# Kernel tuning notes

Measured on AMD Instinct MI355X. Metric: run time of the kernel, lower is better.

## Reference

```python
import jax, jax.numpy as jnp
import numpy as np

N = 100000          # total nodes
G = 128             # number of graphs
D_IN, D_H, D_OUT = 512, 1024, 512
E = 1600000         # edges (unused by the math, matches forward signature)


def setup_inputs() -> dict:
    key = jax.random.key(0)
    ks = jax.random.split(key, 9)
    x = jax.random.normal(ks[0], (N, D_IN), dtype=jnp.float32)
    edge_index = jax.random.randint(ks[1], (2, E), 0, N, dtype=jnp.int64)
    # sorted batch ids; guarantee every graph id appears at least once
    batch = jnp.sort(jnp.concatenate([
        jnp.arange(G, dtype=jnp.int64),
        jax.random.randint(ks[2], (N - G,), 0, G, dtype=jnp.int64),
    ]))
    s = 0.02
    W0 = jax.random.normal(ks[3], (D_IN, D_H), dtype=jnp.float32) * s
    b0 = jnp.zeros((D_H,), dtype=jnp.float32)
    W1 = jax.random.normal(ks[4], (D_H, D_H), dtype=jnp.float32) * s
    b1 = jnp.zeros((D_H,), dtype=jnp.float32)
    W2 = jax.random.normal(ks[5], (D_H, D_OUT), dtype=jnp.float32) * s
    b2 = jnp.zeros((D_OUT,), dtype=jnp.float32)
    return {"x": x, "edge_index": edge_index, "batch": batch,
            "W0": W0, "b0": b0, "W1": W1, "b1": b1, "W2": W2, "b2": b2}


def reference(x, edge_index, batch, W0, b0, W1, b1, W2, b2):
    # Linear + ReLU stack (dropout p=0 -> identity in eval). edge_index is unused,
    # matching the original module (its 'GCN' layer is a plain nn.Linear).
    h = jax.nn.relu(x @ W0 + b0)
    h = jax.nn.relu(h @ W1 + b1)
    h = jax.nn.relu(h @ W2 + b2)        # [N, D_OUT]
    # global mean pool per graph: fused segment-sum replaces the per-graph mask loop
    sums = jax.ops.segment_sum(h, batch, num_segments=G)                 # [G, D_OUT]
    counts = jax.ops.segment_sum(jnp.ones((h.shape[0],), h.dtype), batch,
                                 num_segments=G)                          # [G]
    return sums / counts[:, None]
```

## Files before the change

kernel.cpp:

```cpp
#include <hip/hip_runtime.h>
#include <cstdint>
#include <cstddef>

typedef __bf16 bf16x8 __attribute__((ext_vector_type(8)));
typedef float f32x4 __attribute__((ext_vector_type(4)));

__device__ __forceinline__ unsigned short f2bf(float f) {
  unsigned u = __float_as_uint(f);
  u += 0x7fffu + ((u >> 16) & 1u);
  return (unsigned short)(u >> 16);
}
__device__ __forceinline__ float bf2f(unsigned short s) {
  return __uint_as_float(((unsigned)s) << 16);
}

__device__ __forceinline__ void gld_lds16(const void* g, void* l) {
  __builtin_amdgcn_global_load_lds(
      (const __attribute__((address_space(1))) void*)g,
      (__attribute__((address_space(3))) void*)l, 16, 0, 0);
}

#define BARM() do { __builtin_amdgcn_s_barrier(); asm volatile("" ::: "memory"); } while (0)
#define VMCNT(n) asm volatile("s_waitcnt vmcnt(" #n ")" ::: "memory")

__global__ void transpose_w(const float* __restrict__ w, unsigned short* __restrict__ wt,
                            int K, int N) {
  __shared__ float tile[32][33];
  int nt = N >> 5;
  int bx = blockIdx.x % nt;
  int by = blockIdx.x / nt;
  int tx = threadIdx.x & 31, ty = threadIdx.x >> 5;
#pragma unroll
  for (int r = 0; r < 32; r += 8)
    tile[ty + r][tx] = w[(size_t)(by * 32 + ty + r) * N + bx * 32 + tx];
  __syncthreads();
#pragma unroll
  for (int r = 0; r < 32; r += 8)
    wt[(size_t)(bx * 32 + ty + r) * K + by * 32 + tx] = f2bf(tile[tx][ty + r]);
}

__global__ void cvt_x(const float* __restrict__ x, unsigned short* __restrict__ xb,
                      int rows, int nvalid, int D) {
  size_t total = (size_t)rows * D / 8;
  for (size_t i = (size_t)blockIdx.x * blockDim.x + threadIdx.x; i < total;
       i += (size_t)gridDim.x * blockDim.x) {
    size_t e = i * 8;
    int row = (int)(e / (size_t)D);
    uint4 ov;
    if (row < nvalid) {
      const float4* s = (const float4*)(x + e);
      float4 v0 = s[0], v1 = s[1];
      ov.x = (unsigned)f2bf(v0.x) | ((unsigned)f2bf(v0.y) << 16);
      ov.y = (unsigned)f2bf(v0.z) | ((unsigned)f2bf(v0.w) << 16);
      ov.z = (unsigned)f2bf(v1.x) | ((unsigned)f2bf(v1.y) << 16);
      ov.w = (unsigned)f2bf(v1.z) | ((unsigned)f2bf(v1.w) << 16);
    } else {
      ov.x = ov.y = ov.z = ov.w = 0u;
    }
    *(uint4*)(xb + e) = ov;
  }
}

__device__ __forceinline__ bf16x8 read_frag(const unsigned short* region, int row, int kel) {
  int ke = kel ^ (((row >> 1) & 3) << 3);
  return *(const bf16x8*)(region + row * 32 + ke);
}

__device__ __forceinline__ void stage_half(const unsigned short* gpanel, int K, int kofs,
                                           unsigned short* region, int tid) {
#pragma unroll
  for (int r = 0; r < 2; ++r) {
    int row = r * 128 + (tid >> 2);
    int ke = ((tid & 3) * 8) ^ (((row >> 1) & 3) << 3);
    gld_lds16(gpanel + (size_t)row * K + kofs + ke, region + r * 4096 + tid * 8);
  }
}

#define MFMA16(MB, BV)                                                          \
  do {                                                                          \
    __builtin_amdgcn_s_setprio(1);                                              \
    _Pragma("unroll") for (int mm = 0; mm < 4; ++mm) {                          \
      _Pragma("unroll") for (int nn = 0; nn < 4; ++nn)                          \
        acc[(MB) + mm][nn] = __builtin_amdgcn_mfma_f32_16x16x32_bf16(           \
            av[mm], BV[nn], acc[(MB) + mm][nn], 0, 0, 0);                       \
    }                                                                           \
    __builtin_amdgcn_s_setprio(0);                                              \
  } while (0)

__global__ __launch_bounds__(512, 2) void gemm256(
    const unsigned short* __restrict__ A,
    const unsigned short* __restrict__ Bt,
    const float* __restrict__ bias,
    unsigned short* __restrict__ C,
    int N, int K) {
  __shared__ alignas(16) unsigned short lds[2][2][2][256][32];
  const int tid = threadIdx.x;
  const int w = tid >> 6, l = tid & 63;
  const int wm = w >> 2, wn = w & 3;
  const int lc = l & 15, lk8 = (l >> 4) * 8;

  const int nbn = N >> 8;
  const int nwg = gridDim.x;
  const int q = nwg >> 3, rr = nwg & 7;
  const int xcd = blockIdx.x & 7, ib = blockIdx.x >> 3;
  const int swz = (xcd < rr ? xcd * (q + 1) : rr * (q + 1) + (xcd - rr) * q) + ib;
  const int bm = swz / nbn, bn = swz - bm * nbn;

  const unsigned short* Ap = A + (size_t)bm * 256 * K;
  const unsigned short* Bp = Bt + (size_t)bn * 256 * K;
  const int T = K >> 6;

  f32x4 acc[8][4] = {};

  stage_half(Ap, K, 0, &lds[0][0][0][0][0], tid);
  stage_half(Bp, K, 0, &lds[0][1][0][0][0], tid);
  stage_half(Ap, K, 32, &lds[0][0][1][0][0], tid);
  stage_half(Bp, K, 32, &lds[0][1][1][0][0], tid);
  stage_half(Ap, K, 64, &lds[1][0][0][0][0], tid);
  stage_half(Bp, K, 64, &lds[1][1][0][0][0], tid);
  VMCNT(4);
  BARM();

  for (int t = 0; t < T; ++t) {
    const int s = t & 1;
    const unsigned short* Ak0 = &lds[s][0][0][0][0];
    const unsigned short* Ak1 = &lds[s][0][1][0][0];
    const unsigned short* Bk0 = &lds[s][1][0][0][0];
    const unsigned short* Bk1 = &lds[s][1][1][0][0];
    unsigned short* nAk1 = &lds[s ^ 1][0][1][0][0];
    unsigned short* nBk1 = &lds[s ^ 1][1][1][0][0];
    unsigned short* cAk0 = &lds[s][0][0][0][0];
    unsigned short* cBk0 = &lds[s][1][0][0][0];
    bf16x8 av[4], b0[4], b1[4];

#pragma unroll
    for (int mm = 0; mm < 4; ++mm) av[mm] = read_frag(Ak0, wm * 128 + mm * 16 + lc, lk8);
#pragma unroll
    for (int nn = 0; nn < 4; ++nn) b0[nn] = read_frag(Bk0, wn * 64 + nn * 16 + lc, lk8);
    if (t + 1 < T) stage_half(Ap, K, (t + 1) * 64 + 32, nAk1, tid);
    BARM();
    MFMA16(0, b0);
    BARM();

#pragma unroll
    for (int mm = 0; mm < 4; ++mm) av[mm] = read_frag(Ak0, wm * 128 + (4 + mm) * 16 + lc, lk8);
    if (t + 1 < T) stage_half(Bp, K, (t + 1) * 64 + 32, nBk1, tid);
    BARM();
    MFMA16(4, b0);
    BARM();

#pragma unroll
    for (int mm = 0; mm < 4; ++mm) av[mm] = read_frag(Ak1, wm * 128 + mm * 16 + lc, lk8);
#pragma unroll
    for (int nn = 0; nn < 4; ++nn) b1[nn] = read_frag(Bk1, wn * 64 + nn * 16 + lc, lk8);
    if (t + 2 < T) stage_half(Ap, K, (t + 2) * 64, cAk0, tid);
    BARM();
    MFMA16(0, b1);
    BARM();

#pragma unroll
    for (int mm = 0; mm < 4; ++mm) av[mm] = read_frag(Ak1, wm * 128 + (4 + mm) * 16 + lc, lk8);
    if (t + 2 < T) {
      stage_half(Bp, K, (t + 2) * 64, cBk0, tid);
      VMCNT(4);
    } else {
      VMCNT(0);
    }
    BARM();
    MFMA16(4, b1);
    BARM();
  }

#pragma unroll
  for (int nn = 0; nn < 4; ++nn) {
    int col = bn * 256 + wn * 64 + nn * 16 + lc;
    float bv = bias[col];
#pragma unroll
    for (int mm = 0; mm < 8; ++mm) {
      size_t rowb = (size_t)bm * 256 + wm * 128 + mm * 16 + (l >> 4) * 4;
#pragma unroll
      for (int j = 0; j < 4; ++j) {
        float v = fmaxf(acc[mm][nn][j] + bv, 0.0f);
        C[(rowb + j) * N + col] = f2bf(v);
      }
    }
  }
}

__global__ void pool_partial(const unsigned short* __restrict__ h2, const int* __restrict__ batch,
                             float* __restrict__ part, int n, int D, int S) {
  int g = blockIdx.x / S, sub = blockIdx.x - g * S;
  int lo, hi;
  { int a = 0, b = n; while (a < b) { int m = (a + b) >> 1; if (batch[m] < g) a = m + 1; else b = m; } lo = a; }
  { int a = lo, b = n; while (a < b) { int m = (a + b) >> 1; if (batch[m] < g + 1) a = m + 1; else b = m; } hi = a; }
  int t = threadIdx.x;
  float sx = 0.f, sy = 0.f;
  for (int r = lo + sub; r < hi; r += S) {
    unsigned v = *(const unsigned*)(h2 + (size_t)r * D + t * 2);
    sx += bf2f((unsigned short)(v & 0xffffu));
    sy += bf2f((unsigned short)(v >> 16));
  }
  float* o = part + (size_t)blockIdx.x * D + t * 2;
  o[0] = sx;
  o[1] = sy;
}

__global__ void pool_reduce(const float* __restrict__ part, const int* __restrict__ batch,
                            float* __restrict__ out, int n, int D, int S, int G) {
  int idx = blockIdx.x * blockDim.x + threadIdx.x;
  if (idx >= G * D) return;
  int g = idx / D, d = idx - g * D;
  int lo, hi;
  { int a = 0, b = n; while (a < b) { int m = (a + b) >> 1; if (batch[m] < g) a = m + 1; else b = m; } lo = a; }
  { int a = lo, b = n; while (a < b) { int m = (a + b) >> 1; if (batch[m] < g + 1) a = m + 1; else b = m; } hi = a; }
  float sum = 0.f;
  for (int k = 0; k < S; ++k) sum += part[(size_t)(g * S + k) * D + d];
  out[idx] = sum / (float)(hi - lo);
}

static inline size_t align256(size_t x) { return (x + 255) & ~(size_t)255; }

extern "C" void kernel_launch(void* const* d_in, const int* in_sizes, int n_in,
                              void* d_out, int out_size, void* d_ws, size_t ws_size,
                              hipStream_t stream) {
  const float* x = (const float*)d_in[0];
  const int* batch = (const int*)d_in[2];
  const float* W0 = (const float*)d_in[3];
  const float* b0 = (const float*)d_in[4];
  const float* W1 = (const float*)d_in[5];
  const float* b1 = (const float*)d_in[6];
  const float* W2 = (const float*)d_in[7];
  const float* b2 = (const float*)d_in[8];
  float* out = (float*)d_out;

  const int Nn = in_sizes[2];
  const int DIN = 512, DH = 1024, DOUT = 512;
  const int G = out_size / DOUT;
  const int S = 8;
  const int Mpad = ((Nn + 255) / 256) * 256;

  uint8_t* p = (uint8_t*)d_ws;
  unsigned short* W0t = (unsigned short*)p; p += align256((size_t)DH * DIN * 2);
  unsigned short* W1t = (unsigned short*)p; p += align256((size_t)DH * DH * 2);
  unsigned short* W2t = (unsigned short*)p; p += align256((size_t)DOUT * DH * 2);
  unsigned short* h2  = (unsigned short*)p; p += align256((size_t)Mpad * DOUT * 2);
  float* part         = (float*)p;          p += align256((size_t)G * S * DOUT * 4);
  size_t used = (size_t)(p - (uint8_t*)d_ws);
  size_t avail = ws_size > used ? ws_size - used : 0;
  size_t per_row = (size_t)(DIN + DH + DH) * 2;
  long long chl = (long long)(avail / per_row);
  chl = (chl / 256) * 256;
  int CH = (int)(chl < 256 ? 256 : chl);
  if (CH > Mpad) CH = Mpad;
  unsigned short* xb = (unsigned short*)p; p += align256((size_t)CH * DIN * 2);
  unsigned short* h0 = (unsigned short*)p; p += align256((size_t)CH * DH * 2);
  unsigned short* h1 = (unsigned short*)p; p += align256((size_t)CH * DH * 2);

  transpose_w<<<dim3((DIN / 32) * (DH / 32)), 256, 0, stream>>>(W0, W0t, DIN, DH);
  transpose_w<<<dim3((DH / 32) * (DH / 32)), 256, 0, stream>>>(W1, W1t, DH, DH);
  transpose_w<<<dim3((DH / 32) * (DOUT / 32)), 256, 0, stream>>>(W2, W2t, DH, DOUT);

  for (int off = 0; off < Mpad; off += CH) {
    int rows = Mpad - off; if (rows > CH) rows = CH;
    int nvalid = Nn - off;
    size_t cvt_threads = (size_t)rows * DIN / 8;
    int cvt_blocks = (int)((cvt_threads + 255) / 256);
    if (cvt_blocks > 2048) cvt_blocks = 2048;
    cvt_x<<<dim3(cvt_blocks), 256, 0, stream>>>(x + (size_t)off * DIN, xb, rows, nvalid, DIN);

    gemm256<<<dim3((rows / 256) * (DH / 256)), 512, 0, stream>>>(xb, W0t, b0, h0, DH, DIN);
    gemm256<<<dim3((rows / 256) * (DH / 256)), 512, 0, stream>>>(h0, W1t, b1, h1, DH, DH);
    gemm256<<<dim3((rows / 256) * (DOUT / 256)), 512, 0, stream>>>(
        h1, W2t, b2, h2 + (size_t)off * DOUT, DOUT, DH);
  }

  pool_partial<<<dim3(G * S), 256, 0, stream>>>(h2, batch, part, Nn, DOUT, S);
  pool_reduce<<<dim3((G * DOUT + 255) / 256), 256, 0, stream>>>(part, batch, out, Nn, DOUT, S, G);
}
```

Before: 735.0 us.

## Stage GEMM epilogue through swizzled LDS for 16-byte coalesced stores; add lgkmcnt waits

```diff
diff --git a/kernel.cpp b/kernel.cpp
--- a/kernel.cpp
+++ b/kernel.cpp
@@ -22,6 +22,8 @@
 
 #define BARM() do { __builtin_amdgcn_s_barrier(); asm volatile("" ::: "memory"); } while (0)
 #define VMCNT(n) asm volatile("s_waitcnt vmcnt(" #n ")" ::: "memory")
+#define LGKM0()  do { asm volatile("s_waitcnt lgkmcnt(0)" ::: "memory"); \
+                      __builtin_amdgcn_sched_barrier(0); } while (0)
 
 __global__ void transpose_w(const float* __restrict__ w, unsigned short* __restrict__ wt,
                             int K, int N) {
@@ -103,8 +105,8 @@
   const int nwg = gridDim.x;
   const int q = nwg >> 3, rr = nwg & 7;
   const int xcd = blockIdx.x & 7, ib = blockIdx.x >> 3;
-  const int swz = (xcd < rr ? xcd * (q + 1) : rr * (q + 1) + (xcd - rr) * q) + ib;
-  const int bm = swz / nbn, bn = swz - bm * nbn;
+  const int bswz = (xcd < rr ? xcd * (q + 1) : rr * (q + 1) + (xcd - rr) * q) + ib;
+  const int bm = bswz / nbn, bn = bswz - bm * nbn;
 
   const unsigned short* Ap = A + (size_t)bm * 256 * K;
   const unsigned short* Bp = Bt + (size_t)bn * 256 * K;
@@ -139,6 +141,7 @@
     for (int nn = 0; nn < 4; ++nn) b0[nn] = read_frag(Bk0, wn * 64 + nn * 16 + lc, lk8);
     if (t + 1 < T) stage_half(Ap, K, (t + 1) * 64 + 32, nAk1, tid);
     BARM();
+    LGKM0();
     MFMA16(0, b0);
     BARM();
 
@@ -146,6 +149,7 @@
     for (int mm = 0; mm < 4; ++mm) av[mm] = read_frag(Ak0, wm * 128 + (4 + mm) * 16 + lc, lk8);
     if (t + 1 < T) stage_half(Bp, K, (t + 1) * 64 + 32, nBk1, tid);
     BARM();
+    LGKM0();
     MFMA16(4, b0);
     BARM();
 
@@ -155,6 +159,7 @@
     for (int nn = 0; nn < 4; ++nn) b1[nn] = read_frag(Bk1, wn * 64 + nn * 16 + lc, lk8);
     if (t + 2 < T) stage_half(Ap, K, (t + 2) * 64, cAk0, tid);
     BARM();
+    LGKM0();
     MFMA16(0, b1);
     BARM();
 
@@ -167,23 +172,43 @@
       VMCNT(0);
     }
     BARM();
+    LGKM0();
     MFMA16(4, b1);
     BARM();
   }
 
-#pragma unroll
-  for (int nn = 0; nn < 4; ++nn) {
-    int col = bn * 256 + wn * 64 + nn * 16 + lc;
-    float bv = bias[col];
-#pragma unroll
-    for (int mm = 0; mm < 8; ++mm) {
-      size_t rowb = (size_t)bm * 256 + wm * 128 + mm * 16 + (l >> 4) * 4;
-#pragma unroll
-      for (int j = 0; j < 4; ++j) {
-        float v = fmaxf(acc[mm][nn][j] + bv, 0.0f);
-        C[(rowb + j) * N + col] = f2bf(v);
+  unsigned short* eps = &lds[0][0][0][0][0];
+  float bv[4];
+#pragma unroll
+  for (int nn = 0; nn < 4; ++nn) bv[nn] = bias[bn * 256 + wn * 64 + nn * 16 + lc];
+
+#pragma unroll
+  for (int r = 0; r < 2; ++r) {
+    if (wm == r) {
+#pragma unroll
+      for (int mm = 0; mm < 8; ++mm) {
+#pragma unroll
+        for (int nn = 0; nn < 4; ++nn) {
+          int lcol = wn * 64 + nn * 16 + lc;
+#pragma unroll
+          for (int j = 0; j < 4; ++j) {
+            int lrow = mm * 16 + (l >> 4) * 4 + j;
+            float v = fmaxf(acc[mm][nn][j] + bv[nn], 0.0f);
+            eps[lrow * 256 + (lcol ^ (((lrow >> 2) & 3) << 4))] = f2bf(v);
+          }
+        }
       }
     }
+    BARM();
+#pragma unroll
+    for (int it = 0; it < 8; ++it) {
+      int flat = it * 512 + tid;
+      int lrow = flat >> 5, cb = flat & 31;
+      int ce = (cb * 8) ^ (((lrow >> 2) & 3) << 4);
+      uint4 v = *(const uint4*)&eps[lrow * 256 + ce];
+      *(uint4*)&C[(size_t)(bm * 256 + r * 128 + lrow) * N + bn * 256 + cb * 8] = v;
+    }
+    BARM();
   }
 }
 
```

Measured after the change: 709.5 us. 1.04x faster.
